# Kernel tuning notes

Hardware: AMD Instinct MI355X
Metric: run time of the kernel (lower is better)

The kernel has to match this reference:

```python
import jax, jax.numpy as jnp
import numpy as np

B, D, H, O, R = 128, 1024, 131072, 1024, 512


def setup_inputs() -> dict:
    key = jax.random.key(0)
    k1, k2, k3 = jax.random.split(key, 3)
    x = jax.random.normal(k1, (B, D), dtype=jnp.float32)
    # xavier-uniform-like scale for in_weight [hidden, input]
    W_in = jax.random.normal(k2, (H, D), dtype=jnp.float32) * (1.0 / np.sqrt(D))
    # out_weight = randn * 0.1 per the module
    W_out = jax.random.normal(k3, (H, O), dtype=jnp.float32) * 0.1
    return {"x": x, "W_in": W_in, "W_out": W_out, "sparsity_dim": R}


def reference(x, W_in, W_out, sparsity_dim):
    # Exact inner-product retrieval (reference for CAGRA ANN, metric='inner_product')
    scores_BH = jnp.einsum('bd,hd->bh', x, W_in)          # (B, H)
    _, idx_BR = jax.lax.top_k(scores_BH, sparsity_dim)    # (B, R) indices into memory
    keys_BRD = W_in[idx_BR]                               # (B, R, D) gathered key rows
    vals_BRO = W_out[idx_BR]                              # (B, R, O) gathered value rows
    coeff_BR = jnp.einsum('bd,brd->br', x, keys_BRD)      # bmm(x, keys^T)
    out_BO = jnp.einsum('br,bro->bo', jax.nn.gelu(coeff_BR, approximate=False), vals_BRO)
    return out_BO
```

## Files before the change

### kernel.cpp

```cpp
#include <hip/hip_runtime.h>
#include <math.h>

typedef unsigned int u32;
typedef unsigned long long u64;
typedef _Float16 f16;
typedef f16 half8v __attribute__((ext_vector_type(8)));
typedef float f32x4 __attribute__((ext_vector_type(4)));

#define Bc 128
#define Dc 1024
#define Hc 131072
#define Oc 1024
#define Rc 512

#define NBINS 4096
#define NSUB 2
#define CAP 6144

#define WS_SCORES ((size_t)0)
#define WS_THR    ((size_t)Bc * Hc)
#define WS_SEL    (WS_THR + (size_t)Bc * 4)
#define WS_PART   (WS_SEL + (size_t)Bc * Rc)
#define WS_XHI    (WS_PART + (size_t)Bc * 4 * Oc)
#define WS_XLO    (WS_XHI + (size_t)Bc * Dc / 2)

__device__ __forceinline__ u32 mono_key(float f) {
    u32 u = __float_as_uint(f);
    return (u & 0x80000000u) ? ~u : (u | 0x80000000u);
}

__global__ __launch_bounds__(512) void kx_split(const float* __restrict__ x,
                                                f16* __restrict__ xhi,
                                                f16* __restrict__ xlo) {
    int c = blockIdx.x * 512 + threadIdx.x;
    int row = c >> 7;
    int kc = c & 127;
    const float* src = x + (size_t)row * Dc + kc * 8;
    float4 v0 = *reinterpret_cast<const float4*>(src);
    float4 v1 = *reinterpret_cast<const float4*>(src + 4);
    int kt = kc >> 2;
    int kslot = kc & 3;
    int dst = kt * 4096 + row * 32 + ((kslot ^ (row & 3)) << 3);
    half8v h, l;
#pragma unroll
    for (int e = 0; e < 8; ++e) {
        float f = (e < 4) ? reinterpret_cast<const float*>(&v0)[e]
                          : reinterpret_cast<const float*>(&v1)[e - 4];
        f16 hh = (f16)f;
        h[e] = hh;
        l[e] = (f16)((f - (float)hh) * 2048.0f);
    }
    *reinterpret_cast<half8v*>(xhi + dst) = h;
    *reinterpret_cast<half8v*>(xlo + dst) = l;
}

#define AHI 0
#define ALO 4096
#define BHI 8192
#define BLO 12288
__global__ __launch_bounds__(512) void k1_mfma(const float* __restrict__ Win,
                                               const f16* __restrict__ xhi,
                                               const f16* __restrict__ xlo,
                                               float* __restrict__ S) {
    __shared__ f16 lds[2][16384];
    const int tid = threadIdx.x;
    const int h0 = blockIdx.x * 128;
    const int brow = tid >> 2;
    const int bslot = tid & 3;
    const float* bsrc = Win + (size_t)(h0 + brow) * Dc + bslot * 8;
    const int wB = brow * 32 + ((bslot ^ (brow & 3)) << 3);

    const int lane = tid & 63;
    const int wid = tid >> 6;
    const int wm = wid >> 2;
    const int wn = wid & 3;
    const int lr = lane & 15;
    const int lk = lane >> 4;

    f32x4 acc1[4][2], acc2[4][2];
#pragma unroll
    for (int i = 0; i < 4; ++i)
#pragma unroll
        for (int j = 0; j < 2; ++j) {
            acc1[i][j] = (f32x4){0.f, 0.f, 0.f, 0.f};
            acc2[i][j] = (f32x4){0.f, 0.f, 0.f, 0.f};
        }

    {
        float4 vb0 = *reinterpret_cast<const float4*>(bsrc);
        float4 vb1 = *reinterpret_cast<const float4*>(bsrc + 4);
        half8v ha = *reinterpret_cast<const half8v*>(xhi + tid * 8);
        half8v la = *reinterpret_cast<const half8v*>(xlo + tid * 8);
        half8v bh, bl;
#pragma unroll
        for (int e = 0; e < 8; ++e) {
            float f = (e < 4) ? reinterpret_cast<const float*>(&vb0)[e]
                              : reinterpret_cast<const float*>(&vb1)[e - 4];
            f16 hh = (f16)f;
            bh[e] = hh;
            bl[e] = (f16)((f - (float)hh) * 2048.0f);
        }
        f16* L = lds[0];
        *reinterpret_cast<half8v*>(L + AHI + tid * 8) = ha;
        *reinterpret_cast<half8v*>(L + ALO + tid * 8) = la;
        *reinterpret_cast<half8v*>(L + BHI + wB) = bh;
        *reinterpret_cast<half8v*>(L + BLO + wB) = bl;
    }
    __syncthreads();

    for (int ks = 0; ks < 32; ++ks) {
        f16* C = lds[ks & 1];
        f16* N = lds[(ks & 1) ^ 1];
        const bool pf = (ks < 31);
        float4 nvb0, nvb1;
        half8v nha, nla;
        if (pf) {
            nvb0 = *reinterpret_cast<const float4*>(bsrc + (ks + 1) * 32);
            nvb1 = *reinterpret_cast<const float4*>(bsrc + (ks + 1) * 32 + 4);
            nha = *reinterpret_cast<const half8v*>(xhi + (ks + 1) * 4096 + tid * 8);
            nla = *reinterpret_cast<const half8v*>(xlo + (ks + 1) * 4096 + tid * 8);
        }
        half8v afh[4], afl[4];
#pragma unroll
        for (int i = 0; i < 4; ++i) {
            int r = wm * 64 + i * 16 + lr;
            int ad = r * 32 + ((lk ^ (r & 3)) << 3);
            afh[i] = *reinterpret_cast<const half8v*>(C + AHI + ad);
            afl[i] = *reinterpret_cast<const half8v*>(C + ALO + ad);
        }
#pragma unroll
        for (int j = 0; j < 2; ++j) {
            int cdx = wn * 32 + j * 16 + lr;
            int bd = cdx * 32 + ((lk ^ (cdx & 3)) << 3);
            half8v bfh = *reinterpret_cast<const half8v*>(C + BHI + bd);
            half8v bfl = *reinterpret_cast<const half8v*>(C + BLO + bd);
#pragma unroll
            for (int i = 0; i < 4; ++i) {
                acc1[i][j] = __builtin_amdgcn_mfma_f32_16x16x32_f16(afh[i], bfh, acc1[i][j], 0, 0, 0);
                acc2[i][j] = __builtin_amdgcn_mfma_f32_16x16x32_f16(afh[i], bfl, acc2[i][j], 0, 0, 0);
                acc2[i][j] = __builtin_amdgcn_mfma_f32_16x16x32_f16(afl[i], bfh, acc2[i][j], 0, 0, 0);
            }
        }
        if (pf) {
            half8v bh, bl;
#pragma unroll
            for (int e = 0; e < 8; ++e) {
                float f = (e < 4) ? reinterpret_cast<const float*>(&nvb0)[e]
                                  : reinterpret_cast<const float*>(&nvb1)[e - 4];
                f16 hh = (f16)f;
                bh[e] = hh;
                bl[e] = (f16)((f - (float)hh) * 2048.0f);
            }
            *reinterpret_cast<half8v*>(N + AHI + tid * 8) = nha;
            *reinterpret_cast<half8v*>(N + ALO + tid * 8) = nla;
            *reinterpret_cast<half8v*>(N + BHI + wB) = bh;
            *reinterpret_cast<half8v*>(N + BLO + wB) = bl;
            __syncthreads();
        }
    }
#pragma unroll
    for (int i = 0; i < 4; ++i)
#pragma unroll
        for (int j = 0; j < 2; ++j)
#pragma unroll
            for (int r = 0; r < 4; ++r) {
                int row = wm * 64 + i * 16 + lk * 4 + r;
                int col = h0 + wn * 32 + j * 16 + lr;
                S[(size_t)row * Hc + col] = acc1[i][j][r] + acc2[i][j][r] * (1.0f / 2048.0f);
            }
}

#define K2_LDS_BYTES ((NSUB * NBINS) * 4 + Rc * 8 + CAP * 8)
__global__ __launch_bounds__(1024) void k2_select(const float* __restrict__ S,
                                                  u32* __restrict__ selidx) {
    extern __shared__ u32 dyn[];
    u32* lh  = dyn;
    u64* top = (u64*)(dyn + NSUB * NBINS);
    u64* cand = (u64*)(dyn + NSUB * NBINS + Rc * 2);
    __shared__ u32 csum[64];
    __shared__ u32 s_bint, s_need, cnt_top, cnt_cand;

    const int b = blockIdx.x;
    const int tid = threadIdx.x;
    for (int i = tid; i < NSUB * NBINS; i += 1024) lh[i] = 0;
    if (tid == 0) { cnt_top = 0; cnt_cand = 0; }
    __syncthreads();

    const float4* row4 = reinterpret_cast<const float4*>(S + (size_t)b * Hc);
    const int sub = (tid & (NSUB - 1)) * NBINS;
    for (int it = 0; it < Hc / 4096; ++it) {
        float4 v = row4[tid + it * 1024];
#pragma unroll
        for (int e = 0; e < 4; ++e) {
            u32 bin = mono_key(reinterpret_cast<const float*>(&v)[e]) >> 20;
            atomicAdd(&lh[sub + bin], 1u);
        }
    }
    __syncthreads();
    for (int i = tid; i < NBINS; i += 1024) lh[i] += lh[NBINS + i];
    __syncthreads();
    if (tid < 64) {
        u32 s = 0;
        for (int j = 0; j < 64; ++j) s += lh[tid * 64 + j];
        csum[tid] = s;
    }
    __syncthreads();
    if (tid == 0) {
        u32 cum = 0;
        int c;
        for (c = 63; c >= 0; --c) {
            if (cum + csum[c] >= (u32)Rc) break;
            cum += csum[c];
        }
        int bin_t = 0; u32 above = 0;
        for (int j = 63; j >= 0; --j) {
            int bin = c * 64 + j;
            if (cum + lh[bin] >= (u32)Rc) { bin_t = bin; above = cum; break; }
            cum += lh[bin];
        }
        s_bint = (u32)bin_t;
        s_need = (u32)Rc - above;
    }
    __syncthreads();
    const u32 bin_t = s_bint;
    const u32 need  = s_need;
    for (int it = 0; it < Hc / 4096; ++it) {
        float4 v = row4[tid + it * 1024];
        int i0 = (tid + it * 1024) * 4;
#pragma unroll
        for (int e = 0; e < 4; ++e) {
            u32 u = mono_key(reinterpret_cast<const float*>(&v)[e]);
            u32 bin = u >> 20;
            if (bin > bin_t) {
                u32 p = atomicAdd(&cnt_top, 1u);
                top[p] = ((u64)u << 32) | (u64)(0xFFFFFFFFu - (u32)(i0 + e));
            } else if (bin == bin_t) {
                u32 p = atomicAdd(&cnt_cand, 1u);
                if (p < CAP) cand[p] = ((u64)u << 32) | (u64)(0xFFFFFFFFu - (u32)(i0 + e));
            }
        }
    }
    __syncthreads();
    const int ntop = (int)cnt_top;
    const int nc   = (int)(cnt_cand < (u32)CAP ? cnt_cand : (u32)CAP);
    u32* sel = selidx + (size_t)b * Rc;
    for (int j = tid; j < ntop; j += 1024) {
        u64 my = top[j];
        u32 r = 0;
        for (int k = 0; k < ntop; ++k) r += (top[k] > my) ? 1u : 0u;
        sel[r] = 0xFFFFFFFFu - (u32)(my & 0xFFFFFFFFu);
    }
    for (int j = tid; j < nc; j += 1024) {
        u64 my = cand[j];
        u32 r = 0;
        for (int k = 0; k < nc; ++k) r += (cand[k] > my) ? 1u : 0u;
        if (r < need) sel[ntop + r] = 0xFFFFFFFFu - (u32)(my & 0xFFFFFFFFu);
    }
}

__global__ __launch_bounds__(256) void k3_gather(const float* __restrict__ S,
                                                 const float* __restrict__ Wout,
                                                 const u32* __restrict__ selidx,
                                                 float* __restrict__ part) {
    __shared__ float g[128];
    __shared__ u32 il[128];
    const int b  = blockIdx.x >> 2;
    const int ch = blockIdx.x & 3;
    const int tid = threadIdx.x;
    if (tid < 128) {
        u32 idx = selidx[(size_t)b * Rc + ch * 128 + tid];
        il[tid] = idx;
        float s = S[(size_t)b * Hc + idx];
        g[tid] = 0.5f * s * (1.0f + erff(s * 0.70710678118654752f));
    }
    __syncthreads();
    float4 acc = make_float4(0.f, 0.f, 0.f, 0.f);
    const int o0 = tid * 4;
#pragma unroll 4
    for (int j = 0; j < 128; ++j) {
        float w = g[j];
        float4 v = *reinterpret_cast<const float4*>(&Wout[(size_t)il[j] * Oc + o0]);
        acc.x = fmaf(w, v.x, acc.x);
        acc.y = fmaf(w, v.y, acc.y);
        acc.z = fmaf(w, v.z, acc.z);
        acc.w = fmaf(w, v.w, acc.w);
    }
    *reinterpret_cast<float4*>(&part[((size_t)b * 4 + ch) * Oc + o0]) = acc;
}

__global__ __launch_bounds__(256) void k4_reduce(const float* __restrict__ part,
                                                 float* __restrict__ out) {
    const int b = blockIdx.x;
    const int o0 = threadIdx.x * 4;
    float4 a = *reinterpret_cast<const float4*>(&part[((size_t)b * 4 + 0) * Oc + o0]);
    float4 c1 = *reinterpret_cast<const float4*>(&part[((size_t)b * 4 + 1) * Oc + o0]);
    float4 c2 = *reinterpret_cast<const float4*>(&part[((size_t)b * 4 + 2) * Oc + o0]);
    float4 c3 = *reinterpret_cast<const float4*>(&part[((size_t)b * 4 + 3) * Oc + o0]);
    a.x += c1.x + c2.x + c3.x;
    a.y += c1.y + c2.y + c3.y;
    a.z += c1.z + c2.z + c3.z;
    a.w += c1.w + c2.w + c3.w;
    *reinterpret_cast<float4*>(&out[(size_t)b * Oc + o0]) = a;
}

extern "C" void kernel_launch(void* const* d_in, const int* in_sizes, int n_in,
                              void* d_out, int out_size, void* d_ws, size_t ws_size,
                              hipStream_t stream) {
    (void)in_sizes; (void)n_in; (void)out_size; (void)ws_size;
    const float* x    = (const float*)d_in[0];
    const float* Win  = (const float*)d_in[1];
    const float* Wout = (const float*)d_in[2];
    float* out = (float*)d_out;

    float* S    = (float*)d_ws + WS_SCORES;
    u32*   sel  = (u32*)d_ws + WS_SEL;
    float* part = (float*)d_ws + WS_PART;
    f16*   xhi  = (f16*)((u32*)d_ws + WS_XHI);
    f16*   xlo  = (f16*)((u32*)d_ws + WS_XLO);

    static bool attr_set = false;
    if (!attr_set) {
        hipFuncSetAttribute((const void*)k2_select,
                            hipFuncAttributeMaxDynamicSharedMemorySize, K2_LDS_BYTES);
        attr_set = true;
    }

    kx_split<<<32, 512, 0, stream>>>(x, xhi, xlo);
    k1_mfma<<<Hc / 128, 512, 0, stream>>>(Win, xhi, xlo, S);
    k2_select<<<Bc, 1024, K2_LDS_BYTES, stream>>>(S, sel);
    k3_gather<<<Bc * 4, 256, 0, stream>>>(S, Wout, sel, part);
    k4_reduce<<<Bc, 256, 0, stream>>>(part, out);
}
```

Measured before the change: 263.8 us.

## Halve k1 block size, widen warp tiles, load x tiles via direct global-to-LDS DMA

The scoring GEMM kernel now runs 256-thread blocks with each wave computing a 64x64 tile instead of 64x32, and launch bounds ask for two blocks per CU. The pre-split x hi/lo tiles are copied straight into LDS with global_load_lds instead of passing through registers. Each thread now converts 16 W_in floats per k-step rather than 8. This trades more accumulator registers per thread for fewer LDS fragment reloads per MFMA and less register traffic for the A operand. The unused threshold workspace slot is removed.

```diff
diff --git a/kernel.cpp b/kernel.cpp
--- a/kernel.cpp
+++ b/kernel.cpp
@@ -18,8 +18,7 @@
 #define CAP 6144
 
 #define WS_SCORES ((size_t)0)
-#define WS_THR    ((size_t)Bc * Hc)
-#define WS_SEL    (WS_THR + (size_t)Bc * 4)
+#define WS_SEL    ((size_t)Bc * Hc)
 #define WS_PART   (WS_SEL + (size_t)Bc * Rc)
 #define WS_XHI    (WS_PART + (size_t)Bc * 4 * Oc)
 #define WS_XLO    (WS_XHI + (size_t)Bc * Dc / 2)
@@ -27,6 +26,12 @@
 __device__ __forceinline__ u32 mono_key(float f) {
     u32 u = __float_as_uint(f);
     return (u & 0x80000000u) ? ~u : (u | 0x80000000u);
+}
+
+__device__ __forceinline__ void dma16(const f16* gsrc, const f16* ldst) {
+    __builtin_amdgcn_global_load_lds(
+        (const __attribute__((address_space(1))) unsigned int*)(const void*)gsrc,
+        (__attribute__((address_space(3))) unsigned int*)(const void*)ldst, 16, 0, 0);
 }
 
 __global__ __launch_bounds__(512) void kx_split(const float* __restrict__ x,
@@ -58,53 +63,69 @@
 #define ALO 4096
 #define BHI 8192
 #define BLO 12288
-__global__ __launch_bounds__(512) void k1_mfma(const float* __restrict__ Win,
-                                               const f16* __restrict__ xhi,
-                                               const f16* __restrict__ xlo,
-                                               float* __restrict__ S) {
+__global__ __launch_bounds__(256, 2) void k1_mfma(const float* __restrict__ Win,
+                                                  const f16* __restrict__ xhi,
+                                                  const f16* __restrict__ xlo,
+                                                  float* __restrict__ S) {
     __shared__ f16 lds[2][16384];
     const int tid = threadIdx.x;
     const int h0 = blockIdx.x * 128;
-    const int brow = tid >> 2;
-    const int bslot = tid & 3;
-    const float* bsrc = Win + (size_t)(h0 + brow) * Dc + bslot * 8;
-    const int wB = brow * 32 + ((bslot ^ (brow & 3)) << 3);
+
+    const int bcol = tid >> 1;
+    const int bkh = tid & 1;
+    const float* bsrc = Win + (size_t)(h0 + bcol) * Dc + bkh * 16;
+    const int bs0 = bcol * 32 + (((bkh * 2 + 0) ^ (bcol & 3)) << 3);
+    const int bs1 = bcol * 32 + (((bkh * 2 + 1) ^ (bcol & 3)) << 3);
 
     const int lane = tid & 63;
     const int wid = tid >> 6;
-    const int wm = wid >> 2;
-    const int wn = wid & 3;
+    const int wm = wid >> 1;
+    const int wn = wid & 1;
     const int lr = lane & 15;
     const int lk = lane >> 4;
-
-    f32x4 acc1[4][2], acc2[4][2];
+    const int dmaoff = wid * 512;
+
+    f32x4 acc1[4][4], acc2[4][4];
 #pragma unroll
     for (int i = 0; i < 4; ++i)
 #pragma unroll
-        for (int j = 0; j < 2; ++j) {
+        for (int j = 0; j < 4; ++j) {
             acc1[i][j] = (f32x4){0.f, 0.f, 0.f, 0.f};
             acc2[i][j] = (f32x4){0.f, 0.f, 0.f, 0.f};
         }
 
     {
-        float4 vb0 = *reinterpret_cast<const float4*>(bsrc);
-        float4 vb1 = *reinterpret_cast<const float4*>(bsrc + 4);
-        half8v ha = *reinterpret_cast<const half8v*>(xhi + tid * 8);
-        half8v la = *reinterpret_cast<const half8v*>(xlo + tid * 8);
-        half8v bh, bl;
+        f16* L = lds[0];
+        dma16(xhi + 0 * 4096 + 0 + dmaoff + lane * 8, L + AHI + 0 + dmaoff);
+        dma16(xhi + 0 * 4096 + 2048 + dmaoff + lane * 8, L + AHI + 2048 + dmaoff);
+        dma16(xlo + 0 * 4096 + 0 + dmaoff + lane * 8, L + ALO + 0 + dmaoff);
+        dma16(xlo + 0 * 4096 + 2048 + dmaoff + lane * 8, L + ALO + 2048 + dmaoff);
+        float4 q0 = *reinterpret_cast<const float4*>(bsrc);
+        float4 q1 = *reinterpret_cast<const float4*>(bsrc + 4);
+        float4 q2 = *reinterpret_cast<const float4*>(bsrc + 8);
+        float4 q3 = *reinterpret_cast<const float4*>(bsrc + 12);
+        half8v h0, l0, h1, l1;
 #pragma unroll
         for (int e = 0; e < 8; ++e) {
-            float f = (e < 4) ? reinterpret_cast<const float*>(&vb0)[e]
-                              : reinterpret_cast<const float*>(&vb1)[e - 4];
-            f16 hh = (f16)f;
-            bh[e] = hh;
-            bl[e] = (f16)((f - (float)hh) * 2048.0f);
-        }
-        f16* L = lds[0];
-        *reinterpret_cast<half8v*>(L + AHI + tid * 8) = ha;
-        *reinterpret_cast<half8v*>(L + ALO + tid * 8) = la;
-        *reinterpret_cast<half8v*>(L + BHI + wB) = bh;
-        *reinterpret_cast<half8v*>(L + BLO + wB) = bl;
+            float fa = reinterpret_cast<const float*>(&q0)[e < 4 ? e : -1];
+            (void)fa;
+        }
+#pragma unroll
+        for (int e = 0; e < 4; ++e) {
+            float f;
+            f = reinterpret_cast<const float*>(&q0)[e];
+            { f16 hh = (f16)f; h0[e] = hh; l0[e] = (f16)((f - (float)hh) * 2048.0f); }
+            f = reinterpret_cast<const float*>(&q1)[e];
+            { f16 hh = (f16)f; h0[e + 4] = hh; l0[e + 4] = (f16)((f - (float)hh) * 2048.0f); }
+            f = reinterpret_cast<const float*>(&q2)[e];
+            { f16 hh = (f16)f; h1[e] = hh; l1[e] = (f16)((f - (float)hh) * 2048.0f); }
+            f = reinterpret_cast<const float*>(&q3)[e];
+            { f16 hh = (f16)f; h1[e + 4] = hh; l1[e + 4] = (f16)((f - (float)hh) * 2048.0f); }
+        }
+        *reinterpret_cast<half8v*>(L + BHI + bs0) = h0;
+        *reinterpret_cast<half8v*>(L + BLO + bs0) = l0;
+        *reinterpret_cast<half8v*>(L + BHI + bs1) = h1;
+        *reinterpret_cast<half8v*>(L + BLO + bs1) = l1;
     }
     __syncthreads();
 
@@ -112,13 +133,19 @@
         f16* C = lds[ks & 1];
         f16* N = lds[(ks & 1) ^ 1];
         const bool pf = (ks < 31);
-        float4 nvb0, nvb1;
-        half8v nha, nla;
+        float4 q0, q1, q2, q3;
         if (pf) {
-            nvb0 = *reinterpret_cast<const float4*>(bsrc + (ks + 1) * 32);
-            nvb1 = *reinterpret_cast<const float4*>(bsrc + (ks + 1) * 32 + 4);
-            nha = *reinterpret_cast<const half8v*>(xhi + (ks + 1) * 4096 + tid * 8);
-            nla = *reinterpret_cast<const half8v*>(xlo + (ks + 1) * 4096 + tid * 8);
+            const float* bs = bsrc + (ks + 1) * 32;
+            q0 = *reinterpret_cast<const float4*>(bs);
+            q1 = *reinterpret_cast<const float4*>(bs + 4);
+            q2 = *reinterpret_cast<const float4*>(bs + 8);
+            q3 = *reinterpret_cast<const float4*>(bs + 12);
+            const f16* xh = xhi + (ks + 1) * 4096;
+            const f16* xl = xlo + (ks + 1) * 4096;
+            dma16(xh + 0 + dmaoff + lane * 8, N + AHI + 0 + dmaoff);
+            dma16(xh + 2048 + dmaoff + lane * 8, N + AHI + 2048 + dmaoff);
+            dma16(xl + 0 + dmaoff + lane * 8, N + ALO + 0 + dmaoff);
+            dma16(xl + 2048 + dmaoff + lane * 8, N + ALO + 2048 + dmaoff);
         }
         half8v afh[4], afl[4];
 #pragma unroll
@@ -129,8 +156,8 @@
             afl[i] = *reinterpret_cast<const half8v*>(C + ALO + ad);
         }
 #pragma unroll
-        for (int j = 0; j < 2; ++j) {
-            int cdx = wn * 32 + j * 16 + lr;
+        for (int j = 0; j < 4; ++j) {
+            int cdx = wn * 64 + j * 16 + lr;
             int bd = cdx * 32 + ((lk ^ (cdx & 3)) << 3);
             half8v bfh = *reinterpret_cast<const half8v*>(C + BHI + bd);
             half8v bfl = *reinterpret_cast<const half8v*>(C + BLO + bd);
@@ -142,30 +169,34 @@
             }
         }
         if (pf) {
-            half8v bh, bl;
-#pragma unroll
-            for (int e = 0; e < 8; ++e) {
-                float f = (e < 4) ? reinterpret_cast<const float*>(&nvb0)[e]
-                                  : reinterpret_cast<const float*>(&nvb1)[e - 4];
-                f16 hh = (f16)f;
-                bh[e] = hh;
-                bl[e] = (f16)((f - (float)hh) * 2048.0f);
+            half8v h0, l0, h1, l1;
+#pragma unroll
+            for (int e = 0; e < 4; ++e) {
+                float f;
+                f = reinterpret_cast<const float*>(&q0)[e];
+                { f16 hh = (f16)f; h0[e] = hh; l0[e] = (f16)((f - (float)hh) * 2048.0f); }
+                f = reinterpret_cast<const float*>(&q1)[e];
+                { f16 hh = (f16)f; h0[e + 4] = hh; l0[e + 4] = (f16)((f - (float)hh) * 2048.0f); }
+                f = reinterpret_cast<const float*>(&q2)[e];
+                { f16 hh = (f16)f; h1[e] = hh; l1[e] = (f16)((f - (float)hh) * 2048.0f); }
+                f = reinterpret_cast<const float*>(&q3)[e];
+                { f16 hh = (f16)f; h1[e + 4] = hh; l1[e + 4] = (f16)((f - (float)hh) * 2048.0f); }
             }
-            *reinterpret_cast<half8v*>(N + AHI + tid * 8) = nha;
-            *reinterpret_cast<half8v*>(N + ALO + tid * 8) = nla;
-            *reinterpret_cast<half8v*>(N + BHI + wB) = bh;
-            *reinterpret_cast<half8v*>(N + BLO + wB) = bl;
-            __syncthreads();
-        }
+            *reinterpret_cast<half8v*>(N + BHI + bs0) = h0;
+            *reinterpret_cast<half8v*>(N + BLO + bs0) = l0;
+            *reinterpret_cast<half8v*>(N + BHI + bs1) = h1;
+            *reinterpret_cast<half8v*>(N + BLO + bs1) = l1;
+        }
+        __syncthreads();
     }
 #pragma unroll
     for (int i = 0; i < 4; ++i)
 #pragma unroll
-        for (int j = 0; j < 2; ++j)
+        for (int j = 0; j < 4; ++j)
 #pragma unroll
             for (int r = 0; r < 4; ++r) {
                 int row = wm * 64 + i * 16 + lk * 4 + r;
-                int col = h0 + wn * 32 + j * 16 + lr;
+                int col = h0 + wn * 64 + j * 16 + lr;
                 S[(size_t)row * Hc + col] = acc1[i][j][r] + acc2[i][j][r] * (1.0f / 2048.0f);
             }
 }
@@ -326,7 +357,7 @@
     }
 
     kx_split<<<32, 512, 0, stream>>>(x, xhi, xlo);
-    k1_mfma<<<Hc / 128, 512, 0, stream>>>(Win, xhi, xlo, S);
+    k1_mfma<<<Hc / 128, 256, 0, stream>>>(Win, xhi, xlo, S);
     k2_select<<<Bc, 1024, K2_LDS_BYTES, stream>>>(S, sel);
     k3_gather<<<Bc * 4, 256, 0, stream>>>(S, Wout, sel, part);
     k4_reduce<<<Bc, 256, 0, stream>>>(part, out);
```

Result: no change. 265.5 us (+0.6%).

## Stream GEMM tiles into LDS via async global_load_lds with 4-stage ring

Applied to the files above, without the earlier changes.

Rewrites the score GEMM kernel to load x splits and raw fp32 W_in tiles straight into LDS with global_load_lds DMA, using a 4-buffer ring that prefetches two stages ahead and uses manual vmcnt waits. Blocks drop to 256 threads, so each wave computes a 64x64 tile instead of 64x32. The fp32-to-f16 hi/lo split of W_in moves from the staging step to after the LDS read. The aim is to hide global latency and cut register traffic, at the cost of 128KB of LDS per block, which limits occupancy, and of redundant conversion work per wave.

```diff
diff --git a/kernel.cpp b/kernel.cpp
--- a/kernel.cpp
+++ b/kernel.cpp
@@ -18,8 +18,7 @@
 #define CAP 6144
 
 #define WS_SCORES ((size_t)0)
-#define WS_THR    ((size_t)Bc * Hc)
-#define WS_SEL    (WS_THR + (size_t)Bc * 4)
+#define WS_SEL    ((size_t)Bc * Hc)
 #define WS_PART   (WS_SEL + (size_t)Bc * Rc)
 #define WS_XHI    (WS_PART + (size_t)Bc * 4 * Oc)
 #define WS_XLO    (WS_XHI + (size_t)Bc * Dc / 2)
@@ -27,6 +26,12 @@
 __device__ __forceinline__ u32 mono_key(float f) {
     u32 u = __float_as_uint(f);
     return (u & 0x80000000u) ? ~u : (u | 0x80000000u);
+}
+
+__device__ __forceinline__ void dma16(const void* gsrc, void* ldst) {
+    __builtin_amdgcn_global_load_lds(
+        (const __attribute__((address_space(1))) unsigned int*)gsrc,
+        (__attribute__((address_space(3))) unsigned int*)ldst, 16, 0, 0);
 }
 
 __global__ __launch_bounds__(512) void kx_split(const float* __restrict__ x,
@@ -38,9 +43,7 @@
     const float* src = x + (size_t)row * Dc + kc * 8;
     float4 v0 = *reinterpret_cast<const float4*>(src);
     float4 v1 = *reinterpret_cast<const float4*>(src + 4);
-    int kt = kc >> 2;
-    int kslot = kc & 3;
-    int dst = kt * 4096 + row * 32 + ((kslot ^ (row & 3)) << 3);
+    int dst = (kc >> 2) * 4096 + row * 32 + (kc & 3) * 8;
     half8v h, l;
 #pragma unroll
     for (int e = 0; e < 8; ++e) {
@@ -54,86 +57,101 @@
     *reinterpret_cast<half8v*>(xlo + dst) = l;
 }
 
-#define AHI 0
-#define ALO 4096
-#define BHI 8192
-#define BLO 12288
-__global__ __launch_bounds__(512) void k1_mfma(const float* __restrict__ Win,
+#define NT 32
+#define BUFSZ 32768
+#define K1_LDS_BYTES (4 * BUFSZ)
+__global__ __launch_bounds__(256) void k1_mfma(const float* __restrict__ Win,
                                                const f16* __restrict__ xhi,
                                                const f16* __restrict__ xlo,
                                                float* __restrict__ S) {
-    __shared__ f16 lds[2][16384];
+    extern __shared__ char k1lds[];
     const int tid = threadIdx.x;
     const int h0 = blockIdx.x * 128;
-    const int brow = tid >> 2;
-    const int bslot = tid & 3;
-    const float* bsrc = Win + (size_t)(h0 + brow) * Dc + bslot * 8;
-    const int wB = brow * 32 + ((bslot ^ (brow & 3)) << 3);
-
     const int lane = tid & 63;
     const int wid = tid >> 6;
-    const int wm = wid >> 2;
-    const int wn = wid & 3;
+    const int wm = wid >> 1;
+    const int wn = wid & 1;
     const int lr = lane & 15;
     const int lk = lane >> 4;
 
-    f32x4 acc1[4][2], acc2[4][2];
+    const int ar0 = wid * 16 + (lane >> 2);
+    const int ar1 = 64 + ar0;
+    const int asp = lane & 3;
+    const int aoff0 = ar0 * 32 + ((asp ^ ((ar0 >> 1) & 3)) << 3);
+    const int aoff1 = ar1 * 32 + ((asp ^ ((ar1 >> 1) & 3)) << 3);
+    const int bgd = lane & 7;
+    int bco[4];
+#pragma unroll
+    for (int s = 0; s < 4; ++s) {
+        int col = s * 32 + wid * 8 + (lane >> 3);
+        bco[s] = (h0 + col) * Dc + ((bgd ^ (col & 7)) << 2);
+    }
+    const int dq = wid * 1024;
+
+#define STAGE(KT, Q) do {                                                   \
+        char* nb_ = k1lds + (Q) * BUFSZ;                                    \
+        dma16(xhi + (KT) * 4096 + aoff0, nb_ + 0    + dq);                  \
+        dma16(xhi + (KT) * 4096 + aoff1, nb_ + 4096 + dq);                  \
+        dma16(xlo + (KT) * 4096 + aoff0, nb_ + 8192 + dq);                  \
+        dma16(xlo + (KT) * 4096 + aoff1, nb_ + 12288 + dq);                 \
+        dma16(Win + bco[0] + (KT) * 32, nb_ + 16384 + dq);                  \
+        dma16(Win + bco[1] + (KT) * 32, nb_ + 20480 + dq);                  \
+        dma16(Win + bco[2] + (KT) * 32, nb_ + 24576 + dq);                  \
+        dma16(Win + bco[3] + (KT) * 32, nb_ + 28672 + dq);                  \
+    } while (0)
+
+    f32x4 acc1[4][4], acc2[4][4];
 #pragma unroll
     for (int i = 0; i < 4; ++i)
 #pragma unroll
-        for (int j = 0; j < 2; ++j) {
+        for (int j = 0; j < 4; ++j) {
             acc1[i][j] = (f32x4){0.f, 0.f, 0.f, 0.f};
             acc2[i][j] = (f32x4){0.f, 0.f, 0.f, 0.f};
         }
 
-    {
-        float4 vb0 = *reinterpret_cast<const float4*>(bsrc);
-        float4 vb1 = *reinterpret_cast<const float4*>(bsrc + 4);
-        half8v ha = *reinterpret_cast<const half8v*>(xhi + tid * 8);
-        half8v la = *reinterpret_cast<const half8v*>(xlo + tid * 8);
-        half8v bh, bl;
-#pragma unroll
-        for (int e = 0; e < 8; ++e) {
-            float f = (e < 4) ? reinterpret_cast<const float*>(&vb0)[e]
-                              : reinterpret_cast<const float*>(&vb1)[e - 4];
-            f16 hh = (f16)f;
-            bh[e] = hh;
-            bl[e] = (f16)((f - (float)hh) * 2048.0f);
-        }
-        f16* L = lds[0];
-        *reinterpret_cast<half8v*>(L + AHI + tid * 8) = ha;
-        *reinterpret_cast<half8v*>(L + ALO + tid * 8) = la;
-        *reinterpret_cast<half8v*>(L + BHI + wB) = bh;
-        *reinterpret_cast<half8v*>(L + BLO + wB) = bl;
-    }
-    __syncthreads();
-
-    for (int ks = 0; ks < 32; ++ks) {
-        f16* C = lds[ks & 1];
-        f16* N = lds[(ks & 1) ^ 1];
-        const bool pf = (ks < 31);
-        float4 nvb0, nvb1;
-        half8v nha, nla;
-        if (pf) {
-            nvb0 = *reinterpret_cast<const float4*>(bsrc + (ks + 1) * 32);
-            nvb1 = *reinterpret_cast<const float4*>(bsrc + (ks + 1) * 32 + 4);
-            nha = *reinterpret_cast<const half8v*>(xhi + (ks + 1) * 4096 + tid * 8);
-            nla = *reinterpret_cast<const half8v*>(xlo + (ks + 1) * 4096 + tid * 8);
-        }
+    STAGE(0, 0);
+    STAGE(1, 1);
+
+    for (int ks = 0; ks < NT; ++ks) {
+        if (ks + 2 < NT) {
+            STAGE(ks + 2, (ks + 2) & 3);
+            asm volatile("s_waitcnt vmcnt(16)" ::: "memory");
+        } else if (ks + 2 == NT) {
+            asm volatile("s_waitcnt vmcnt(8)" ::: "memory");
+        } else {
+            asm volatile("s_waitcnt vmcnt(0)" ::: "memory");
+        }
+        __builtin_amdgcn_s_barrier();
+        __builtin_amdgcn_sched_barrier(0);
+
+        char* cb = k1lds + (ks & 3) * BUFSZ;
+        const f16* Ahi = (const f16*)cb;
+        const f16* Alo = (const f16*)(cb + 8192);
+        const float* Bf = (const float*)(cb + 16384);
+
         half8v afh[4], afl[4];
 #pragma unroll
         for (int i = 0; i < 4; ++i) {
             int r = wm * 64 + i * 16 + lr;
-            int ad = r * 32 + ((lk ^ (r & 3)) << 3);
-            afh[i] = *reinterpret_cast<const half8v*>(C + AHI + ad);
-            afl[i] = *reinterpret_cast<const half8v*>(C + ALO + ad);
-        }
-#pragma unroll
-        for (int j = 0; j < 2; ++j) {
-            int cdx = wn * 32 + j * 16 + lr;
-            int bd = cdx * 32 + ((lk ^ (cdx & 3)) << 3);
-            half8v bfh = *reinterpret_cast<const half8v*>(C + BHI + bd);
-            half8v bfl = *reinterpret_cast<const half8v*>(C + BLO + bd);
+            int ad = r * 32 + ((lk ^ ((r >> 1) & 3)) << 3);
+            afh[i] = *reinterpret_cast<const half8v*>(Ahi + ad);
+            afl[i] = *reinterpret_cast<const half8v*>(Alo + ad);
+        }
+#pragma unroll
+        for (int j = 0; j < 4; ++j) {
+            int col = wn * 64 + j * 16 + lr;
+            float4 p0 = *reinterpret_cast<const float4*>(Bf + col * 32 + (((2 * lk) ^ (col & 7)) << 2));
+            float4 p1 = *reinterpret_cast<const float4*>(Bf + col * 32 + (((2 * lk + 1) ^ (col & 7)) << 2));
+            half8v bfh, bfl;
+#pragma unroll
+            for (int e = 0; e < 4; ++e) {
+                float f = reinterpret_cast<const float*>(&p0)[e];
+                f16 hh = (f16)f;
+                bfh[e] = hh; bfl[e] = (f16)((f - (float)hh) * 2048.0f);
+                f = reinterpret_cast<const float*>(&p1)[e];
+                hh = (f16)f;
+                bfh[e + 4] = hh; bfl[e + 4] = (f16)((f - (float)hh) * 2048.0f);
+            }
 #pragma unroll
             for (int i = 0; i < 4; ++i) {
                 acc1[i][j] = __builtin_amdgcn_mfma_f32_16x16x32_f16(afh[i], bfh, acc1[i][j], 0, 0, 0);
@@ -141,31 +159,16 @@
                 acc2[i][j] = __builtin_amdgcn_mfma_f32_16x16x32_f16(afl[i], bfh, acc2[i][j], 0, 0, 0);
             }
         }
-        if (pf) {
-            half8v bh, bl;
-#pragma unroll
-            for (int e = 0; e < 8; ++e) {
-                float f = (e < 4) ? reinterpret_cast<const float*>(&nvb0)[e]
-                                  : reinterpret_cast<const float*>(&nvb1)[e - 4];
-                f16 hh = (f16)f;
-                bh[e] = hh;
-                bl[e] = (f16)((f - (float)hh) * 2048.0f);
-            }
-            *reinterpret_cast<half8v*>(N + AHI + tid * 8) = nha;
-            *reinterpret_cast<half8v*>(N + ALO + tid * 8) = nla;
-            *reinterpret_cast<half8v*>(N + BHI + wB) = bh;
-            *reinterpret_cast<half8v*>(N + BLO + wB) = bl;
-            __syncthreads();
-        }
-    }
+    }
+#undef STAGE
 #pragma unroll
     for (int i = 0; i < 4; ++i)
 #pragma unroll
-        for (int j = 0; j < 2; ++j)
+        for (int j = 0; j < 4; ++j)
 #pragma unroll
             for (int r = 0; r < 4; ++r) {
                 int row = wm * 64 + i * 16 + lk * 4 + r;
-                int col = h0 + wn * 32 + j * 16 + lr;
+                int col = h0 + wn * 64 + j * 16 + lr;
                 S[(size_t)row * Hc + col] = acc1[i][j][r] + acc2[i][j][r] * (1.0f / 2048.0f);
             }
 }
@@ -322,11 +325,13 @@
     if (!attr_set) {
         hipFuncSetAttribute((const void*)k2_select,
                             hipFuncAttributeMaxDynamicSharedMemorySize, K2_LDS_BYTES);
+        hipFuncSetAttribute((const void*)k1_mfma,
+                            hipFuncAttributeMaxDynamicSharedMemorySize, K1_LDS_BYTES);
         attr_set = true;
     }
 
     kx_split<<<32, 512, 0, stream>>>(x, xhi, xlo);
-    k1_mfma<<<Hc / 128, 512, 0, stream>>>(Win, xhi, xlo, S);
+    k1_mfma<<<Hc / 128, 256, K1_LDS_BYTES, stream>>>(Win, xhi, xlo, S);
     k2_select<<<Bc, 1024, K2_LDS_BYTES, stream>>>(S, sel);
     k3_gather<<<Bc * 4, 256, 0, stream>>>(S, Wout, sel, part);
     k4_reduce<<<Bc, 256, 0, stream>>>(part, out);
```

Result: slower. 314.4 us (+19.2%).
